# Optimization experiments

Measured on AMD Instinct MI355X. Metric: run time of the kernel, lower is better.

## Reference

```python
import jax, jax.numpy as jnp
import numpy as np

N_NODES = 40000


def gcn_conv(x, edge_index, W, b, num_nodes):
    """PyG GCNConv: add self-loops, sym-normalize, x @ W.T then scatter-add, + bias."""
    src = edge_index[0]
    dst = edge_index[1]
    loop = jnp.arange(num_nodes, dtype=src.dtype)
    src = jnp.concatenate([src, loop])
    dst = jnp.concatenate([dst, loop])
    # linear transform first (PyG applies lin before propagate)
    h = x @ W.T  # [N, out]
    # symmetric normalization: deg over destination (with self-loops)
    deg = jax.ops.segment_sum(jnp.ones_like(dst, dtype=h.dtype), dst, num_segments=num_nodes)
    dinv = jnp.where(deg > 0, jax.lax.rsqrt(deg), 0.0)
    norm = dinv[src] * dinv[dst]  # [E+N]
    msg = h[src] * norm[:, None]  # gather + scale
    out = jax.ops.segment_sum(msg, dst, num_segments=num_nodes)  # scatter-add
    return out + b


def setup_inputs() -> dict:
    key = jax.random.key(0)
    k1, k2, k3, k4, k5, k6, k7 = jax.random.split(key, 7)
    C, H, F_out = 128, 128, 1
    E = 640000
    x = jax.random.normal(k1, (N_NODES, C), dtype=jnp.float32)
    edge_index = jax.random.randint(k2, (2, E), 0, N_NODES, dtype=jnp.int64)
    # Glorot-ish init for conv weights (PyG lin.weight shape [out, in]), zero bias
    W1 = jax.random.normal(k3, (H, C), dtype=jnp.float32) / np.sqrt(C)
    b1 = jnp.zeros((H,), dtype=jnp.float32)
    W2 = jax.random.normal(k4, (F_out, H), dtype=jnp.float32) / np.sqrt(H)
    b2 = jnp.zeros((F_out,), dtype=jnp.float32)
    return {"x": x, "edge_index": edge_index, "W1": W1, "b1": b1, "W2": W2, "b2": b2}


def reference(x, edge_index, W1, b1, W2, b2):
    h = gcn_conv(x, edge_index, W1, b1, N_NODES)
    h = jax.nn.relu(h)
    out = gcn_conv(h, edge_index, W2, b2, N_NODES)
    return jax.nn.sigmoid(out)
```

## Files before the change

### kernel.cpp

```cpp
#include <hip/hip_runtime.h>
#include <math.h>
#include <stdint.h>

#define FDIM 128
#define CAP 64

typedef __bf16 bf16x8 __attribute__((ext_vector_type(8)));
typedef float f32x4 __attribute__((ext_vector_type(4)));

__device__ __forceinline__ ushort f2bf(float f) {
    uint32_t u = __float_as_uint(f);
    uint32_t r = (u >> 16) & 1;
    return (ushort)((u + 0x7fffu + r) >> 16);
}


__global__ __launch_bounds__(256) void k_zero4(int4* __restrict__ p, int n4) {
    int i = blockIdx.x * blockDim.x + threadIdx.x;
    int stride = gridDim.x * blockDim.x;
    for (; i < n4; i += stride) p[i] = make_int4(0, 0, 0, 0);
}

__global__ __launch_bounds__(256) void k_scatter_ell(const int* __restrict__ src,
                                                     const int* __restrict__ dst,
                                                     int* __restrict__ cnt,
                                                     int* __restrict__ ell, int E) {
    int e = blockIdx.x * blockDim.x + threadIdx.x;
    if (e < E) {
        int d = dst[e];
        int p = atomicAdd(&cnt[d], 1);
        if (p < CAP) ell[(size_t)d * CAP + p] = src[e];
    }
}


#define XS 136

__global__ __launch_bounds__(256) void k_linear1_mfma(const float* __restrict__ x,
                                                      const float* __restrict__ W,
                                                      const int* __restrict__ cnt,
                                                      ushort* __restrict__ h, int n) {
    __shared__ __align__(16) ushort Wl[128 * XS];
    __shared__ __align__(16) ushort Xl[64 * XS];

    int tid = threadIdx.x;
    int node0 = blockIdx.x * 64;

#pragma unroll
    for (int i = 0; i < 16; ++i) {
        int q = tid + i * 256;
        int j = q >> 5;
        int c0 = (q & 31) * 4;
        float4 v = *(const float4*)(W + (size_t)q * 4);
        uint2 p;
        p.x = (uint32_t)f2bf(v.x) | ((uint32_t)f2bf(v.y) << 16);
        p.y = (uint32_t)f2bf(v.z) | ((uint32_t)f2bf(v.w) << 16);
        *(uint2*)&Wl[j * XS + c0] = p;
    }
#pragma unroll
    for (int i = 0; i < 8; ++i) {
        int q = tid + i * 256;
        int r = q >> 5;
        int c0 = (q & 31) * 4;
        int gr = node0 + r;
        float4 v = make_float4(0.f, 0.f, 0.f, 0.f);
        float s = 0.f;
        if (gr < n) {
            v = *(const float4*)(x + (size_t)gr * FDIM + c0);
            s = rsqrtf((float)cnt[gr] + 1.0f);
        }
        uint2 p;
        p.x = (uint32_t)f2bf(v.x * s) | ((uint32_t)f2bf(v.y * s) << 16);
        p.y = (uint32_t)f2bf(v.z * s) | ((uint32_t)f2bf(v.w * s) << 16);
        *(uint2*)&Xl[r * XS + c0] = p;
    }
    __syncthreads();

    int lane = tid & 63, wid = tid >> 6;
    int m0 = (wid >> 1) * 32;
    int j0 = (wid & 1) * 64;
    int lrow = lane & 15, kg = lane >> 4;

    bf16x8 af[2][4];
#pragma unroll
    for (int mt = 0; mt < 2; ++mt)
#pragma unroll
        for (int ks = 0; ks < 4; ++ks)
            af[mt][ks] = *(const bf16x8*)&Xl[(m0 + mt * 16 + lrow) * XS + ks * 32 + kg * 8];

    f32x4 acc[2][4] = {};
#pragma unroll
    for (int jt = 0; jt < 4; ++jt) {
        bf16x8 bfr[4];
#pragma unroll
        for (int ks = 0; ks < 4; ++ks)
            bfr[ks] = *(const bf16x8*)&Wl[(j0 + jt * 16 + lrow) * XS + ks * 32 + kg * 8];
#pragma unroll
        for (int mt = 0; mt < 2; ++mt)
#pragma unroll
            for (int ks = 0; ks < 4; ++ks)
                acc[mt][jt] = __builtin_amdgcn_mfma_f32_16x16x32_bf16(
                    af[mt][ks], bfr[ks], acc[mt][jt], 0, 0, 0);
    }

#pragma unroll
    for (int mt = 0; mt < 2; ++mt)
#pragma unroll
        for (int jt = 0; jt < 4; ++jt)
#pragma unroll
            for (int r = 0; r < 4; ++r) {
                int gi = node0 + m0 + mt * 16 + kg * 4 + r;
                int gj = j0 + jt * 16 + lrow;
                if (gi < n) h[(size_t)gi * FDIM + gj] = f2bf(acc[mt][jt][r]);
            }
}


__device__ __forceinline__ float bf_lo(uint32_t u) { return __uint_as_float(u << 16); }
__device__ __forceinline__ float bf_hi(uint32_t u) { return __uint_as_float(u & 0xFFFF0000u); }

__global__ __launch_bounds__(256) void k_agg1_h2(const uint32_t* __restrict__ h,
                                                 const int* __restrict__ ell,
                                                 const int* __restrict__ cnt,
                                                 const float* __restrict__ b1,
                                                 const float* __restrict__ W2,
                                                 float* __restrict__ h2s, int n) {
    int gtid = blockIdx.x * blockDim.x + threadIdx.x;
    int d = gtid >> 6;
    int lane = threadIdx.x & 63;
    if (d >= n) return;

    int degt = cnt[d];
    int deg = min(degt, CAP);
    int myidx = (lane < deg) ? ell[(size_t)d * CAP + lane] : 0;

    uint32_t u = h[(size_t)d * 64 + lane];
    float a0x = bf_lo(u), a0y = bf_hi(u);
    float a1x = 0.f, a1y = 0.f, a2x = 0.f, a2y = 0.f, a3x = 0.f, a3y = 0.f;

    int k = 0;
    for (; k + 3 < deg; k += 4) {
        int s0 = __shfl(myidx, k);
        int s1 = __shfl(myidx, k + 1);
        int s2 = __shfl(myidx, k + 2);
        int s3 = __shfl(myidx, k + 3);
        uint32_t u0 = h[(size_t)s0 * 64 + lane];
        uint32_t u1 = h[(size_t)s1 * 64 + lane];
        uint32_t u2 = h[(size_t)s2 * 64 + lane];
        uint32_t u3 = h[(size_t)s3 * 64 + lane];
        a0x += bf_lo(u0); a0y += bf_hi(u0);
        a1x += bf_lo(u1); a1y += bf_hi(u1);
        a2x += bf_lo(u2); a2y += bf_hi(u2);
        a3x += bf_lo(u3); a3y += bf_hi(u3);
    }
    for (; k < deg; ++k) {
        int s0 = __shfl(myidx, k);
        uint32_t u0 = h[(size_t)s0 * 64 + lane];
        a0x += bf_lo(u0); a0y += bf_hi(u0);
    }

    float dd = rsqrtf((float)degt + 1.0f);
    float ox = ((a0x + a1x) + (a2x + a3x)) * dd;
    float oy = ((a0y + a1y) + (a2y + a3y)) * dd;

    float2 bb = *(const float2*)(b1 + lane * 2);
    float2 ww = *(const float2*)(W2 + lane * 2);
    float s = fmaxf(ox + bb.x, 0.f) * ww.x + fmaxf(oy + bb.y, 0.f) * ww.y;
#pragma unroll
    for (int o = 32; o; o >>= 1) s += __shfl_down(s, o);
    if (lane == 0) h2s[d] = s * dd;
}


__global__ __launch_bounds__(256) void k_agg2(const float* __restrict__ h2s,
                                              const int* __restrict__ ell,
                                              const int* __restrict__ cnt,
                                              const float* __restrict__ b2,
                                              float* __restrict__ out, int n) {
    int i = blockIdx.x * blockDim.x + threadIdx.x;
    if (i >= n) return;
    int degt = cnt[i];
    int deg = min(degt, CAP);
    float acc = h2s[i];
    const int* row = ell + (size_t)i * CAP;
    for (int k = 0; k < deg; ++k) acc += h2s[row[k]];
    float dd = rsqrtf((float)degt + 1.0f);
    float v = acc * dd + b2[0];
    out[i] = 1.f / (1.f + expf(-v));
}


extern "C" void kernel_launch(void* const* d_in, const int* in_sizes, int n_in,
                              void* d_out, int out_size, void* d_ws, size_t ws_size,
                              hipStream_t stream) {
    const float* x  = (const float*)d_in[0];
    const int*   ei = (const int*)d_in[1];
    const float* W1 = (const float*)d_in[2];
    const float* b1 = (const float*)d_in[3];
    const float* W2 = (const float*)d_in[4];
    const float* b2 = (const float*)d_in[5];

    int n = out_size;
    int E = in_sizes[1] / 2;
    const int* src = ei;
    const int* dst = ei + E;

    char* w = (char*)d_ws;
    int*    cnt  = (int*)w;     w += (size_t)((n + 3) & ~3) * 4;
    int*    ell  = (int*)w;     w += (size_t)n * CAP * 4;
    ushort* h1s  = (ushort*)w;  w += (size_t)n * FDIM * 2;
    float*  h2s  = (float*)w;   w += (size_t)n * 4;

    int n4 = ((n + 3) & ~3) / 4;

    k_zero4<<<40, 256, 0, stream>>>((int4*)cnt, n4);
    k_scatter_ell<<<(E + 255) / 256, 256, 0, stream>>>(src, dst, cnt, ell, E);
    k_linear1_mfma<<<(n + 63) / 64, 256, 0, stream>>>(x, W1, cnt, h1s, n);
    k_agg1_h2<<<(n * 64 + 255) / 256, 256, 0, stream>>>((const uint32_t*)h1s, ell, cnt, b1, W2, h2s, n);
    k_agg2<<<(n + 255) / 256, 256, 0, stream>>>(h2s, ell, cnt, b2, (float*)d_out, n);
}
```

Before: 87.79 us.

## Use 16-bit ELL indices, wave-per-node agg2, deeper gather unroll

Stores neighbor indices as ushort to halve the ELL build and read traffic. The second aggregation assigns a 64-lane wavefront per node, with lanes loading neighbors in parallel and reducing by shuffle, instead of one thread looping. The first aggregation adds an 8-wide gather unroll for more memory-level parallelism. The 16-bit indices assume fewer than 65536 nodes.

```diff
diff --git a/kernel.cpp b/kernel.cpp
--- a/kernel.cpp
+++ b/kernel.cpp
@@ -24,12 +24,12 @@
 __global__ __launch_bounds__(256) void k_scatter_ell(const int* __restrict__ src,
                                                      const int* __restrict__ dst,
                                                      int* __restrict__ cnt,
-                                                     int* __restrict__ ell, int E) {
+                                                     ushort* __restrict__ ell, int E) {
     int e = blockIdx.x * blockDim.x + threadIdx.x;
     if (e < E) {
         int d = dst[e];
         int p = atomicAdd(&cnt[d], 1);
-        if (p < CAP) ell[(size_t)d * CAP + p] = src[e];
+        if (p < CAP) ell[(size_t)d * CAP + p] = (ushort)src[e];
     }
 }
 
@@ -120,7 +120,7 @@
 __device__ __forceinline__ float bf_hi(uint32_t u) { return __uint_as_float(u & 0xFFFF0000u); }
 
 __global__ __launch_bounds__(256) void k_agg1_h2(const uint32_t* __restrict__ h,
-                                                 const int* __restrict__ ell,
+                                                 const ushort* __restrict__ ell,
                                                  const int* __restrict__ cnt,
                                                  const float* __restrict__ b1,
                                                  const float* __restrict__ W2,
@@ -132,36 +132,47 @@
 
     int degt = cnt[d];
     int deg = min(degt, CAP);
-    int myidx = (lane < deg) ? ell[(size_t)d * CAP + lane] : 0;
+    int myidx = (lane < deg) ? (int)ell[(size_t)d * CAP + lane] : 0;
 
     uint32_t u = h[(size_t)d * 64 + lane];
-    float a0x = bf_lo(u), a0y = bf_hi(u);
-    float a1x = 0.f, a1y = 0.f, a2x = 0.f, a2y = 0.f, a3x = 0.f, a3y = 0.f;
+    float ax[8], ay[8];
+    ax[0] = bf_lo(u); ay[0] = bf_hi(u);
+#pragma unroll
+    for (int r = 1; r < 8; ++r) { ax[r] = 0.f; ay[r] = 0.f; }
 
     int k = 0;
+    for (; k + 7 < deg; k += 8) {
+        int s[8];
+        uint32_t uu[8];
+#pragma unroll
+        for (int r = 0; r < 8; ++r) s[r] = __shfl(myidx, k + r);
+#pragma unroll
+        for (int r = 0; r < 8; ++r) uu[r] = h[(size_t)s[r] * 64 + lane];
+#pragma unroll
+        for (int r = 0; r < 8; ++r) { ax[r] += bf_lo(uu[r]); ay[r] += bf_hi(uu[r]); }
+    }
     for (; k + 3 < deg; k += 4) {
-        int s0 = __shfl(myidx, k);
-        int s1 = __shfl(myidx, k + 1);
-        int s2 = __shfl(myidx, k + 2);
-        int s3 = __shfl(myidx, k + 3);
-        uint32_t u0 = h[(size_t)s0 * 64 + lane];
-        uint32_t u1 = h[(size_t)s1 * 64 + lane];
-        uint32_t u2 = h[(size_t)s2 * 64 + lane];
-        uint32_t u3 = h[(size_t)s3 * 64 + lane];
-        a0x += bf_lo(u0); a0y += bf_hi(u0);
-        a1x += bf_lo(u1); a1y += bf_hi(u1);
-        a2x += bf_lo(u2); a2y += bf_hi(u2);
-        a3x += bf_lo(u3); a3y += bf_hi(u3);
+        int s[4];
+        uint32_t uu[4];
+#pragma unroll
+        for (int r = 0; r < 4; ++r) s[r] = __shfl(myidx, k + r);
+#pragma unroll
+        for (int r = 0; r < 4; ++r) uu[r] = h[(size_t)s[r] * 64 + lane];
+#pragma unroll
+        for (int r = 0; r < 4; ++r) { ax[r] += bf_lo(uu[r]); ay[r] += bf_hi(uu[r]); }
     }
     for (; k < deg; ++k) {
         int s0 = __shfl(myidx, k);
         uint32_t u0 = h[(size_t)s0 * 64 + lane];
-        a0x += bf_lo(u0); a0y += bf_hi(u0);
-    }
+        ax[0] += bf_lo(u0); ay[0] += bf_hi(u0);
+    }
+
+    float sx = ((ax[0] + ax[1]) + (ax[2] + ax[3])) + ((ax[4] + ax[5]) + (ax[6] + ax[7]));
+    float sy = ((ay[0] + ay[1]) + (ay[2] + ay[3])) + ((ay[4] + ay[5]) + (ay[6] + ay[7]));
 
     float dd = rsqrtf((float)degt + 1.0f);
-    float ox = ((a0x + a1x) + (a2x + a3x)) * dd;
-    float oy = ((a0y + a1y) + (a2y + a3y)) * dd;
+    float ox = sx * dd;
+    float oy = sy * dd;
 
     float2 bb = *(const float2*)(b1 + lane * 2);
     float2 ww = *(const float2*)(W2 + lane * 2);
@@ -173,20 +184,29 @@
 
 
 __global__ __launch_bounds__(256) void k_agg2(const float* __restrict__ h2s,
-                                              const int* __restrict__ ell,
+                                              const ushort* __restrict__ ell,
                                               const int* __restrict__ cnt,
                                               const float* __restrict__ b2,
                                               float* __restrict__ out, int n) {
-    int i = blockIdx.x * blockDim.x + threadIdx.x;
+    int gtid = blockIdx.x * blockDim.x + threadIdx.x;
+    int i = gtid >> 6;
+    int lane = threadIdx.x & 63;
     if (i >= n) return;
+
     int degt = cnt[i];
     int deg = min(degt, CAP);
-    float acc = h2s[i];
-    const int* row = ell + (size_t)i * CAP;
-    for (int k = 0; k < deg; ++k) acc += h2s[row[k]];
-    float dd = rsqrtf((float)degt + 1.0f);
-    float v = acc * dd + b2[0];
-    out[i] = 1.f / (1.f + expf(-v));
+    float v = 0.f;
+    if (lane < deg) {
+        int s = ell[(size_t)i * CAP + lane];
+        v = h2s[s];
+    }
+#pragma unroll
+    for (int o = 32; o; o >>= 1) v += __shfl_down(v, o);
+    if (lane == 0) {
+        float dd = rsqrtf((float)degt + 1.0f);
+        float r = (h2s[i] + v) * dd + b2[0];
+        out[i] = 1.f / (1.f + expf(-r));
+    }
 }
 
 
@@ -206,10 +226,10 @@
     const int* dst = ei + E;
 
     char* w = (char*)d_ws;
-    int*    cnt  = (int*)w;     w += (size_t)((n + 3) & ~3) * 4;
-    int*    ell  = (int*)w;     w += (size_t)n * CAP * 4;
-    ushort* h1s  = (ushort*)w;  w += (size_t)n * FDIM * 2;
-    float*  h2s  = (float*)w;   w += (size_t)n * 4;
+    int*    cnt = (int*)w;     w += (size_t)((n + 3) & ~3) * 4;
+    ushort* ell = (ushort*)w;  w += (size_t)n * CAP * 2;
+    ushort* h1s = (ushort*)w;  w += (size_t)n * FDIM * 2;
+    float*  h2s = (float*)w;   w += (size_t)n * 4;
 
     int n4 = ((n + 3) & ~3) / 4;
 
@@ -217,5 +237,5 @@
     k_scatter_ell<<<(E + 255) / 256, 256, 0, stream>>>(src, dst, cnt, ell, E);
     k_linear1_mfma<<<(n + 63) / 64, 256, 0, stream>>>(x, W1, cnt, h1s, n);
     k_agg1_h2<<<(n * 64 + 255) / 256, 256, 0, stream>>>((const uint32_t*)h1s, ell, cnt, b1, W2, h2s, n);
-    k_agg2<<<(n + 255) / 256, 256, 0, stream>>>(h2s, ell, cnt, b2, (float*)d_out, n);
-}
+    k_agg2<<<(n * 64 + 255) / 256, 256, 0, stream>>>(h2s, ell, cnt, b2, (float*)d_out, n);
+}
```

Measured after the change: 85.38 us. -2.7%, faster.
